# Optimization experiments

Measured on AMD Instinct MI355X. Metric: run time of the kernel, lower is better.

## Reference

```python
import jax, jax.numpy as jnp
import numpy as np

B, S, H, T = 32, 512, 1024, 32


def setup_inputs() -> dict:
    key = jax.random.key(0)
    ks = jax.random.split(key, 8)
    hidden = jax.random.normal(ks[0], (B, S, H), dtype=jnp.float32)
    W = jax.random.normal(ks[1], (H, T), dtype=jnp.float32) * 0.02
    b = jax.random.normal(ks[2], (T,), dtype=jnp.float32) * 0.02
    start_trans = jax.random.normal(ks[3], (T,), dtype=jnp.float32) * 0.1
    end_trans = jax.random.normal(ks[4], (T,), dtype=jnp.float32) * 0.1
    trans = jax.random.normal(ks[5], (T, T), dtype=jnp.float32) * 0.1
    tags = jax.random.randint(ks[6], (B, S), 0, T, dtype=jnp.int64)
    # variable-length mask: first position always valid (CRF requirement)
    lengths = jax.random.randint(ks[7], (B,), S // 2, S + 1)
    mask = jnp.arange(S)[None, :] < lengths[:, None]  # [B,S] bool
    return {"hidden": hidden, "W": W, "b": b, "start_trans": start_trans,
            "end_trans": end_trans, "trans": trans, "tags": tags, "mask": mask}


def reference(hidden, W, b, start_trans, end_trans, trans, tags, mask):
    # emission = log_softmax(fc(last_hidden_state))  [B,S,T]
    emissions = jax.nn.log_softmax(jnp.einsum('bsh,ht->bst', hidden, W) + b, axis=-1)
    maskf = mask.astype(emissions.dtype)

    # --- numerator: score of the gold tag path ---
    emit_tag = jnp.take_along_axis(emissions, tags[..., None], axis=-1)[..., 0]  # [B,S]
    trans_tag = trans[tags[:, :-1], tags[:, 1:]]                                  # [B,S-1]
    num = (start_trans[tags[:, 0]]
           + (emit_tag * maskf).sum(axis=1)
           + (trans_tag * maskf[:, 1:]).sum(axis=1))
    seq_len = mask.sum(axis=1).astype(jnp.int32)                                  # [B]
    last_tags = jnp.take_along_axis(tags, (seq_len - 1)[:, None].astype(tags.dtype), axis=1)[:, 0]
    num = num + end_trans[last_tags]

    # --- denominator: forward algorithm (masked logsumexp recurrence) ---
    alpha0 = start_trans[None, :] + emissions[:, 0]  # [B,T]

    def step(alpha, inp):
        em_t, m_t = inp  # [B,T], [B]
        nxt = jax.nn.logsumexp(alpha[:, :, None] + trans[None] + em_t[:, None, :], axis=1)
        return jnp.where(m_t[:, None], nxt, alpha), None

    em_rest = jnp.moveaxis(emissions[:, 1:], 1, 0)  # [S-1,B,T]
    m_rest = jnp.moveaxis(mask[:, 1:], 1, 0)        # [S-1,B]
    alpha, _ = jax.lax.scan(step, alpha0, (em_rest, m_rest))
    denom = jax.nn.logsumexp(alpha + end_trans[None], axis=1)  # [B]

    llh = num - denom        # CRF returns per-batch log-likelihood
    return -llh.mean()       # loss = (-crf(...)).mean()
```

## Files before the change

### kernel.cpp

```cpp
#include <hip/hip_runtime.h>
#include <hip/hip_bf16.h>


#define Bb 32
#define Ss 512
#define Hh 1024
#define Tt 32
#define NROWS (Bb*Ss)
#define NCHUNK 32
#define CHUNK_L 16

typedef __attribute__((ext_vector_type(8))) short bf16x8;
typedef __attribute__((ext_vector_type(4))) float f32x4;

__device__ __forceinline__ short f2bf(float f) {
  union { float f; unsigned u; } v; v.f = f;
  unsigned u = v.u;
  return (short)((u + 0x7FFFu + ((u >> 16) & 1u)) >> 16);
}

__global__ __launch_bounds__(1024) void wpack_kernel(
    const float* __restrict__ W, short* __restrict__ Wpk) {
  const int k = threadIdx.x;
#pragma unroll
  for (int t = 0; t < 32; ++t)
    Wpk[t * Hh + k] = f2bf(W[k * 32 + t]);
}

__global__ __launch_bounds__(256) void emis_fused_kernel(
    const float* __restrict__ hidden, const short* __restrict__ Wpk,
    const float* __restrict__ bias, float* __restrict__ logem,
    float* __restrict__ pem) {
  __shared__ float red[4 * 16 * 33];
  const int tid = threadIdx.x;
  const int wv = tid >> 6, lane = tid & 63;
  const int n = lane & 15, q = lane >> 4;
  const int row0 = blockIdx.x * 16;
  const int koff = wv * 256;

  const float* ap = hidden + (size_t)(row0 + n) * Hh + koff + 8 * q;
  const short* bpl = Wpk + n * Hh + koff + 8 * q;
  const short* bpr = Wpk + (16 + n) * Hh + koff + 8 * q;

  f32x4 d0 = {0.f, 0.f, 0.f, 0.f}, d1 = {0.f, 0.f, 0.f, 0.f};

  float4 ha[2], hb[2];
  bf16x8 wl[2], wr[2];
  ha[0] = *(const float4*)(ap);
  hb[0] = *(const float4*)(ap + 4);
  wl[0] = *(const bf16x8*)(bpl);
  wr[0] = *(const bf16x8*)(bpr);

  for (int kc = 0; kc < 8; ++kc) {
    const int cur = kc & 1, nxt = cur ^ 1;
    if (kc + 1 < 8) {
      const int off = (kc + 1) * 32;
      ha[nxt] = *(const float4*)(ap + off);
      hb[nxt] = *(const float4*)(ap + off + 4);
      wl[nxt] = *(const bf16x8*)(bpl + off);
      wr[nxt] = *(const bf16x8*)(bpr + off);
    }
    bf16x8 a;
    a[0] = f2bf(ha[cur].x); a[1] = f2bf(ha[cur].y);
    a[2] = f2bf(ha[cur].z); a[3] = f2bf(ha[cur].w);
    a[4] = f2bf(hb[cur].x); a[5] = f2bf(hb[cur].y);
    a[6] = f2bf(hb[cur].z); a[7] = f2bf(hb[cur].w);
    d0 = __builtin_amdgcn_mfma_f32_16x16x32_bf16(a, wl[cur], d0, 0, 0, 0);
    d1 = __builtin_amdgcn_mfma_f32_16x16x32_bf16(a, wr[cur], d1, 0, 0, 0);
  }

#pragma unroll
  for (int r = 0; r < 4; ++r) {
    red[(wv * 16 + 4 * q + r) * 33 + n] = d0[r];
    red[(wv * 16 + 4 * q + r) * 33 + 16 + n] = d1[r];
  }
  __syncthreads();

  const int row = tid >> 4, c0 = tid & 15, c1 = 16 + c0;
  float v0 = 0.f, v1 = 0.f;
#pragma unroll
  for (int w = 0; w < 4; ++w) {
    v0 += red[(w * 16 + row) * 33 + c0];
    v1 += red[(w * 16 + row) * 33 + c1];
  }
  const float L0 = v0 + bias[c0], L1 = v1 + bias[c1];
  float mx = fmaxf(L0, L1);
#pragma unroll
  for (int d = 8; d >= 1; d >>= 1) mx = fmaxf(mx, __shfl_xor(mx, d, 16));
  float se = __expf(L0 - mx) + __expf(L1 - mx);
#pragma unroll
  for (int d = 8; d >= 1; d >>= 1) se += __shfl_xor(se, d, 16);
  const float corr = mx + __logf(se);
  const float lg0 = L0 - corr, lg1 = L1 - corr;
  const size_t rb = (size_t)(row0 + row) * Tt;
  logem[rb + c0] = lg0;
  logem[rb + c1] = lg1;
  pem[rb + c0] = __expf(lg0);
  pem[rb + c1] = __expf(lg1);
}

__global__ __launch_bounds__(64) void num_kernel(
    const float* __restrict__ logem, const float* __restrict__ start_trans,
    const float* __restrict__ trans, const int* __restrict__ tags,
    const int* __restrict__ mask, float* __restrict__ numb,
    int* __restrict__ lenw) {
  const int b = blockIdx.x;
  const int l = threadIdx.x;
  const int base = b * Ss;
  int lensum = 0;
  float s = 0.f;
#pragma unroll
  for (int k = 0; k < 8; ++k) {
    int ss = l + 64 * k;
    int m = mask[base + ss];
    lensum += m;
    if (m) {
      int tg = tags[base + ss];
      s += logem[(size_t)(base + ss) * Tt + tg];
      if (ss > 0) s += trans[tags[base + ss - 1] * Tt + tg];
    }
  }
#pragma unroll
  for (int d = 32; d >= 1; d >>= 1) {
    s += __shfl_xor(s, d);
    lensum += __shfl_xor(lensum, d);
  }
  if (l == 0) {
    numb[b] = s + start_trans[tags[base]];
    lenw[b] = lensum;
  }
}

__global__ __launch_bounds__(256) void chunk_kernel(
    const float* __restrict__ pem, const float* __restrict__ trans,
    const int* __restrict__ lenw, float* __restrict__ ecT,
    float* __restrict__ moff) {
  __shared__ __align__(16) float Pbuf[4 * 32 * 36];
  const int tid = threadIdx.x;
  const int wv = tid >> 6, lane = tid & 63;
  const int n = lane & 15, q = lane >> 4;
  const int chunk = blockIdx.x * 4 + wv;
  const int b = chunk >> 5, cc = chunk & 31;
  float* P = Pbuf + wv * 32 * 36;

  float etr0[8], etr1[8];
#pragma unroll
  for (int jj = 0; jj < 8; ++jj) {
    etr0[jj] = __expf(trans[(8 * q + jj) * 32 + n]);
    etr1[jj] = __expf(trans[(8 * q + jj) * 32 + 16 + n]);
  }

  const int len = lenw[b];
  const int t0 = 1 + cc * CHUNK_L;
  int nst = (len < Ss ? len : Ss) - t0;
  nst = nst < 0 ? 0 : (nst > CHUNK_L ? CHUNK_L : nst);
  const int rowbase = b * Ss + t0;

  bf16x8 a0, a1;
#pragma unroll
  for (int jj = 0; jj < 8; ++jj) {
    a0[jj] = (n == 8 * q + jj) ? (short)0x3F80 : (short)0;
    a1[jj] = (16 + n == 8 * q + jj) ? (short)0x3F80 : (short)0;
  }

  f32x4 d00, d01, d10, d11;
  if (nst == 0) {
#pragma unroll
    for (int r = 0; r < 4; ++r) {
      d00[r] = (4 * q + r == n) ? 1.f : 0.f;
      d01[r] = 0.f;
      d10[r] = 0.f;
      d11[r] = (4 * q + r == n) ? 1.f : 0.f;
    }
  }
  float em0 = 0.f, em1 = 0.f;
  if (nst > 0) {
    em0 = pem[(size_t)rowbase * Tt + n];
    em1 = pem[(size_t)rowbase * Tt + 16 + n];
  }
  for (int st = 0; st < nst; ++st) {
    float em0n = 0.f, em1n = 0.f;
    if (st + 1 < nst) {
      em0n = pem[(size_t)(rowbase + st + 1) * Tt + n];
      em1n = pem[(size_t)(rowbase + st + 1) * Tt + 16 + n];
    }
    bf16x8 bL, bR;
#pragma unroll
    for (int jj = 0; jj < 8; ++jj) {
      bL[jj] = f2bf(etr0[jj] * em0);
      bR[jj] = f2bf(etr1[jj] * em1);
    }
    const f32x4 z = {0.f, 0.f, 0.f, 0.f};
    d00 = __builtin_amdgcn_mfma_f32_16x16x32_bf16(a0, bL, z, 0, 0, 0);
    d01 = __builtin_amdgcn_mfma_f32_16x16x32_bf16(a0, bR, z, 0, 0, 0);
    d10 = __builtin_amdgcn_mfma_f32_16x16x32_bf16(a1, bL, z, 0, 0, 0);
    d11 = __builtin_amdgcn_mfma_f32_16x16x32_bf16(a1, bR, z, 0, 0, 0);
    if (st + 1 < nst) {
#pragma unroll
      for (int r = 0; r < 4; ++r) {
        P[(4 * q + r) * 36 + n] = d00[r];
        P[(4 * q + r) * 36 + 16 + n] = d01[r];
        P[(16 + 4 * q + r) * 36 + n] = d10[r];
        P[(16 + 4 * q + r) * 36 + 16 + n] = d11[r];
      }
      __builtin_amdgcn_s_waitcnt(0);
      const float4 lo0 = *(const float4*)&P[n * 36 + 8 * q];
      const float4 lo1 = *(const float4*)&P[n * 36 + 8 * q + 4];
      const float4 hi0 = *(const float4*)&P[(16 + n) * 36 + 8 * q];
      const float4 hi1 = *(const float4*)&P[(16 + n) * 36 + 8 * q + 4];
      a0[0] = f2bf(lo0.x); a0[1] = f2bf(lo0.y); a0[2] = f2bf(lo0.z); a0[3] = f2bf(lo0.w);
      a0[4] = f2bf(lo1.x); a0[5] = f2bf(lo1.y); a0[6] = f2bf(lo1.z); a0[7] = f2bf(lo1.w);
      a1[0] = f2bf(hi0.x); a1[1] = f2bf(hi0.y); a1[2] = f2bf(hi0.z); a1[3] = f2bf(hi0.w);
      a1[4] = f2bf(hi1.x); a1[5] = f2bf(hi1.y); a1[6] = f2bf(hi1.z); a1[7] = f2bf(hi1.w);
    }
    em0 = em0n; em1 = em1n;
  }

  float lg0[4], lg1[4], iv0[4], iv1[4];
#pragma unroll
  for (int r = 0; r < 4; ++r) {
    float m0v = fmaxf(d00[r], d01[r]);
    float m1v = fmaxf(d10[r], d11[r]);
#pragma unroll
    for (int d = 8; d >= 1; d >>= 1) {
      m0v = fmaxf(m0v, __shfl_xor(m0v, d, 16));
      m1v = fmaxf(m1v, __shfl_xor(m1v, d, 16));
    }
    m0v = fmaxf(m0v, 1e-37f);
    m1v = fmaxf(m1v, 1e-37f);
    lg0[r] = __logf(m0v); iv0[r] = __builtin_amdgcn_rcpf(m0v);
    lg1[r] = __logf(m1v); iv1[r] = __builtin_amdgcn_rcpf(m1v);
  }
  float* E = ecT + (size_t)(b * NCHUNK + cc) * 32 * 32;
  {
    float4 s;
    s = make_float4(d00[0] * iv0[0], d00[1] * iv0[1], d00[2] * iv0[2], d00[3] * iv0[3]);
    *(float4*)&E[n * 32 + 4 * q] = s;
    s = make_float4(d10[0] * iv1[0], d10[1] * iv1[1], d10[2] * iv1[2], d10[3] * iv1[3]);
    *(float4*)&E[n * 32 + 16 + 4 * q] = s;
    s = make_float4(d01[0] * iv0[0], d01[1] * iv0[1], d01[2] * iv0[2], d01[3] * iv0[3]);
    *(float4*)&E[(16 + n) * 32 + 4 * q] = s;
    s = make_float4(d11[0] * iv1[0], d11[1] * iv1[1], d11[2] * iv1[2], d11[3] * iv1[3]);
    *(float4*)&E[(16 + n) * 32 + 16 + 4 * q] = s;
  }
  if (n == 0) {
    float* Mo = moff + (size_t)(b * NCHUNK + cc) * 32;
    *(float4*)&Mo[4 * q] = make_float4(lg0[0], lg0[1], lg0[2], lg0[3]);
    *(float4*)&Mo[16 + 4 * q] = make_float4(lg1[0], lg1[1], lg1[2], lg1[3]);
  }
}

__global__ __launch_bounds__(64) void phase2_kernel(
    const float* __restrict__ logem, const float* __restrict__ start_trans,
    const float* __restrict__ end_trans, const float* __restrict__ ecT,
    const float* __restrict__ moff, const float* __restrict__ numb,
    const int* __restrict__ lenw, const int* __restrict__ tags,
    float* __restrict__ out) {
  const int b = blockIdx.x;
  const int lane = threadIdx.x;
  const int j = lane & 31;
  __shared__ __align__(16) float qlds[32];

  const float* base = ecT + (size_t)b * NCHUNK * 32 * 32;
  const float* mbase = moff + (size_t)b * NCHUNK * 32;

  float4 M[8], N[8];
  const float* r0 = base + j * 32;
#pragma unroll
  for (int k = 0; k < 8; ++k) M[k] = *(const float4*)(r0 + 4 * k);
  float mo_cur = mbase[j];

  float al0 = start_trans[j] + logem[(size_t)b * Ss * Tt + j];
  float m0 = al0;
#pragma unroll
  for (int d = 16; d >= 1; d >>= 1) m0 = fmaxf(m0, __shfl_xor(m0, d, 32));
  float a = __expf(al0 - m0);
  float Mb = m0;
  const float eend = __expf(end_trans[j]);

  float mo_next = 0.f;
  for (int c = 0; c < NCHUNK; ++c) {
    if (c + 1 < NCHUNK) {
      const float* rn = base + ((c + 1) * 32 + j) * 32;
#pragma unroll
      for (int k = 0; k < 8; ++k) N[k] = *(const float4*)(rn + 4 * k);
      mo_next = mbase[(c + 1) * 32 + j];
    }
    float mom = mo_cur;
#pragma unroll
    for (int d = 16; d >= 1; d >>= 1) mom = fmaxf(mom, __shfl_xor(mom, d, 32));
    float q = a * __expf(mo_cur - mom);
    if (lane < 32) qlds[j] = q;
    __builtin_amdgcn_s_waitcnt(0);
    float s = 0.f;
#pragma unroll
    for (int k = 0; k < 8; ++k) {
      const float4 q4 = *(const float4*)(qlds + 4 * k);
      s = fmaf(q4.x, M[k].x, s);
      s = fmaf(q4.y, M[k].y, s);
      s = fmaf(q4.z, M[k].z, s);
      s = fmaf(q4.w, M[k].w, s);
    }
    float m = s;
#pragma unroll
    for (int d = 16; d >= 1; d >>= 1) m = fmaxf(m, __shfl_xor(m, d, 32));
    m = fmaxf(m, 1e-30f);
    a = s * __builtin_amdgcn_rcpf(m);
    Mb += mom + __logf(m);
#pragma unroll
    for (int k = 0; k < 8; ++k) M[k] = N[k];
    mo_cur = mo_next;
  }
  float z = a * eend;
#pragma unroll
  for (int d = 16; d >= 1; d >>= 1) z += __shfl_xor(z, d, 32);
  if (lane == 0) {
    const int len = lenw[b];
    const float numfull = numb[b] + end_trans[tags[b * Ss + len - 1]];
    const float denom = Mb + __logf(z);
    atomicAdd(out, -(numfull - denom) * (1.0f / 32.0f));
  }
}

extern "C" void kernel_launch(void* const* d_in, const int* in_sizes, int n_in,
                              void* d_out, int out_size, void* d_ws, size_t ws_size,
                              hipStream_t stream) {
  const float* hidden = (const float*)d_in[0];
  const float* W = (const float*)d_in[1];
  const float* bias = (const float*)d_in[2];
  const float* start_trans = (const float*)d_in[3];
  const float* end_trans = (const float*)d_in[4];
  const float* trans = (const float*)d_in[5];
  const int* tags = (const int*)d_in[6];
  const int* mask = (const int*)d_in[7];
  float* out = (float*)d_out;

  float* logem = (float*)d_ws;
  float* pem = logem + (size_t)NROWS * Tt;
  float* ecT = pem + (size_t)NROWS * Tt;
  float* moff = ecT + (size_t)Bb * NCHUNK * 32 * 32;
  float* numb = moff + (size_t)Bb * NCHUNK * 32;
  int* lenw = (int*)(numb + Bb);
  short* Wpk = (short*)(lenw + Bb);

  hipMemsetAsync(out, 0, sizeof(float), stream);
  wpack_kernel<<<1, 1024, 0, stream>>>(W, Wpk);
  emis_fused_kernel<<<NROWS / 16, 256, 0, stream>>>(hidden, Wpk, bias, logem, pem);
  num_kernel<<<Bb, 64, 0, stream>>>(logem, start_trans, trans, tags, mask, numb,
                                    lenw);
  chunk_kernel<<<Bb * NCHUNK / 4, 256, 0, stream>>>(pem, trans, lenw, ecT, moff);
  phase2_kernel<<<Bb, 64, 0, stream>>>(logem, start_trans, end_trans, ecT, moff,
                                       numb, lenw, tags, out);
}
```

Measured before the change: 172.7 us.

## Fold numerator and memset into other kernels, deepen emission prefetch

```diff
diff --git a/kernel.cpp b/kernel.cpp
--- a/kernel.cpp
+++ b/kernel.cpp
@@ -20,8 +20,10 @@
 }
 
 __global__ __launch_bounds__(1024) void wpack_kernel(
-    const float* __restrict__ W, short* __restrict__ Wpk) {
+    const float* __restrict__ W, short* __restrict__ Wpk,
+    float* __restrict__ out) {
   const int k = threadIdx.x;
+  if (k == 0) out[0] = 0.f;
 #pragma unroll
   for (int t = 0; t < 32; ++t)
     Wpk[t * Hh + k] = f2bf(W[k * 32 + t]);
@@ -44,21 +46,27 @@
 
   f32x4 d0 = {0.f, 0.f, 0.f, 0.f}, d1 = {0.f, 0.f, 0.f, 0.f};
 
-  float4 ha[2], hb[2];
-  bf16x8 wl[2], wr[2];
-  ha[0] = *(const float4*)(ap);
-  hb[0] = *(const float4*)(ap + 4);
-  wl[0] = *(const bf16x8*)(bpl);
-  wr[0] = *(const bf16x8*)(bpr);
-
+  float4 ha[4], hb[4];
+  bf16x8 wl[4], wr[4];
+#pragma unroll
+  for (int s = 0; s < 3; ++s) {
+    const int off = s * 32;
+    ha[s] = *(const float4*)(ap + off);
+    hb[s] = *(const float4*)(ap + off + 4);
+    wl[s] = *(const bf16x8*)(bpl + off);
+    wr[s] = *(const bf16x8*)(bpr + off);
+  }
+
+#pragma unroll
   for (int kc = 0; kc < 8; ++kc) {
-    const int cur = kc & 1, nxt = cur ^ 1;
-    if (kc + 1 < 8) {
-      const int off = (kc + 1) * 32;
-      ha[nxt] = *(const float4*)(ap + off);
-      hb[nxt] = *(const float4*)(ap + off + 4);
-      wl[nxt] = *(const bf16x8*)(bpl + off);
-      wr[nxt] = *(const bf16x8*)(bpr + off);
+    const int cur = kc & 3;
+    if (kc + 3 < 8) {
+      const int nx = (kc + 3) & 3;
+      const int off = (kc + 3) * 32;
+      ha[nx] = *(const float4*)(ap + off);
+      hb[nx] = *(const float4*)(ap + off + 4);
+      wl[nx] = *(const bf16x8*)(bpl + off);
+      wr[nx] = *(const bf16x8*)(bpr + off);
     }
     bf16x8 a;
     a[0] = f2bf(ha[cur].x); a[1] = f2bf(ha[cur].y);
@@ -99,41 +107,9 @@
   pem[rb + c1] = __expf(lg1);
 }
 
-__global__ __launch_bounds__(64) void num_kernel(
-    const float* __restrict__ logem, const float* __restrict__ start_trans,
-    const float* __restrict__ trans, const int* __restrict__ tags,
-    const int* __restrict__ mask, float* __restrict__ numb,
-    int* __restrict__ lenw) {
-  const int b = blockIdx.x;
-  const int l = threadIdx.x;
-  const int base = b * Ss;
-  int lensum = 0;
-  float s = 0.f;
-#pragma unroll
-  for (int k = 0; k < 8; ++k) {
-    int ss = l + 64 * k;
-    int m = mask[base + ss];
-    lensum += m;
-    if (m) {
-      int tg = tags[base + ss];
-      s += logem[(size_t)(base + ss) * Tt + tg];
-      if (ss > 0) s += trans[tags[base + ss - 1] * Tt + tg];
-    }
-  }
-#pragma unroll
-  for (int d = 32; d >= 1; d >>= 1) {
-    s += __shfl_xor(s, d);
-    lensum += __shfl_xor(lensum, d);
-  }
-  if (l == 0) {
-    numb[b] = s + start_trans[tags[base]];
-    lenw[b] = lensum;
-  }
-}
-
 __global__ __launch_bounds__(256) void chunk_kernel(
     const float* __restrict__ pem, const float* __restrict__ trans,
-    const int* __restrict__ lenw, float* __restrict__ ecT,
+    const int* __restrict__ mask, float* __restrict__ ecT,
     float* __restrict__ moff) {
   __shared__ __align__(16) float Pbuf[4 * 32 * 36];
   const int tid = threadIdx.x;
@@ -150,11 +126,12 @@
     etr1[jj] = __expf(trans[(8 * q + jj) * 32 + 16 + n]);
   }
 
-  const int len = lenw[b];
   const int t0 = 1 + cc * CHUNK_L;
-  int nst = (len < Ss ? len : Ss) - t0;
-  nst = nst < 0 ? 0 : (nst > CHUNK_L ? CHUNK_L : nst);
   const int rowbase = b * Ss + t0;
+  int pred = 0;
+  if (lane < 16 && t0 + lane < Ss) pred = mask[rowbase + lane];
+  const unsigned long long bal = __ballot(pred != 0);
+  const int nst = __popcll(bal & 0xFFFFull);
 
   bf16x8 a0, a1;
 #pragma unroll
@@ -253,14 +230,34 @@
 __global__ __launch_bounds__(64) void phase2_kernel(
     const float* __restrict__ logem, const float* __restrict__ start_trans,
     const float* __restrict__ end_trans, const float* __restrict__ ecT,
-    const float* __restrict__ moff, const float* __restrict__ numb,
-    const int* __restrict__ lenw, const int* __restrict__ tags,
+    const float* __restrict__ moff, const float* __restrict__ trans,
+    const int* __restrict__ tags, const int* __restrict__ mask,
     float* __restrict__ out) {
   const int b = blockIdx.x;
   const int lane = threadIdx.x;
   const int j = lane & 31;
   __shared__ __align__(16) float qlds[32];
 
+  const int base_row = b * Ss;
+  int lensum = 0;
+  float snum = 0.f;
+#pragma unroll
+  for (int k = 0; k < 8; ++k) {
+    const int ss = lane + 64 * k;
+    const int m = mask[base_row + ss];
+    lensum += m;
+    if (m) {
+      const int tg = tags[base_row + ss];
+      snum += logem[(size_t)(base_row + ss) * Tt + tg];
+      if (ss > 0) snum += trans[tags[base_row + ss - 1] * Tt + tg];
+    }
+  }
+#pragma unroll
+  for (int d = 32; d >= 1; d >>= 1) {
+    snum += __shfl_xor(snum, d);
+    lensum += __shfl_xor(lensum, d);
+  }
+
   const float* base = ecT + (size_t)b * NCHUNK * 32 * 32;
   const float* mbase = moff + (size_t)b * NCHUNK * 32;
 
@@ -270,7 +267,7 @@
   for (int k = 0; k < 8; ++k) M[k] = *(const float4*)(r0 + 4 * k);
   float mo_cur = mbase[j];
 
-  float al0 = start_trans[j] + logem[(size_t)b * Ss * Tt + j];
+  float al0 = start_trans[j] + logem[(size_t)base_row * Tt + j];
   float m0 = al0;
 #pragma unroll
   for (int d = 16; d >= 1; d >>= 1) m0 = fmaxf(m0, __shfl_xor(m0, d, 32));
@@ -289,8 +286,8 @@
     float mom = mo_cur;
 #pragma unroll
     for (int d = 16; d >= 1; d >>= 1) mom = fmaxf(mom, __shfl_xor(mom, d, 32));
-    float q = a * __expf(mo_cur - mom);
-    if (lane < 32) qlds[j] = q;
+    float qv = a * __expf(mo_cur - mom);
+    if (lane < 32) qlds[j] = qv;
     __builtin_amdgcn_s_waitcnt(0);
     float s = 0.f;
 #pragma unroll
@@ -315,8 +312,8 @@
 #pragma unroll
   for (int d = 16; d >= 1; d >>= 1) z += __shfl_xor(z, d, 32);
   if (lane == 0) {
-    const int len = lenw[b];
-    const float numfull = numb[b] + end_trans[tags[b * Ss + len - 1]];
+    const float numfull = snum + start_trans[tags[base_row]] +
+                          end_trans[tags[base_row + lensum - 1]];
     const float denom = Mb + __logf(z);
     atomicAdd(out, -(numfull - denom) * (1.0f / 32.0f));
   }
@@ -339,16 +336,11 @@
   float* pem = logem + (size_t)NROWS * Tt;
   float* ecT = pem + (size_t)NROWS * Tt;
   float* moff = ecT + (size_t)Bb * NCHUNK * 32 * 32;
-  float* numb = moff + (size_t)Bb * NCHUNK * 32;
-  int* lenw = (int*)(numb + Bb);
-  short* Wpk = (short*)(lenw + Bb);
-
-  hipMemsetAsync(out, 0, sizeof(float), stream);
-  wpack_kernel<<<1, 1024, 0, stream>>>(W, Wpk);
+  short* Wpk = (short*)(moff + (size_t)Bb * NCHUNK * 32);
+
+  wpack_kernel<<<1, 1024, 0, stream>>>(W, Wpk, out);
   emis_fused_kernel<<<NROWS / 16, 256, 0, stream>>>(hidden, Wpk, bias, logem, pem);
-  num_kernel<<<Bb, 64, 0, stream>>>(logem, start_trans, trans, tags, mask, numb,
-                                    lenw);
-  chunk_kernel<<<Bb * NCHUNK / 4, 256, 0, stream>>>(pem, trans, lenw, ecT, moff);
+  chunk_kernel<<<Bb * NCHUNK / 4, 256, 0, stream>>>(pem, trans, mask, ecT, moff);
   phase2_kernel<<<Bb, 64, 0, stream>>>(logem, start_trans, end_trans, ecT, moff,
-                                       numb, lenw, tags, out);
-}
+                                       trans, tags, mask, out);
+}
```

After: 169.3 us. About the same (-1.9%).
